# Kernel tuning notes

Hardware: AMD Instinct MI355X
Metric: run time of the kernel (lower is better)

## Reference

```python
import jax, jax.numpy as jnp
import numpy as np

N, E = 100_000, 800_000
D = 100   # memory_dim (in_channels)
T = 100   # time_dim
H, C = 2, 50  # heads, per-head out channels (embedding_dim = H*C = 100)
M = 172   # msg_dim
ED = M + T  # edge_dim for TransformerConv


def setup_inputs() -> dict:
    key = jax.random.key(0)
    ks = jax.random.split(key, 16)
    w = lambda k, shp: jax.random.normal(k, shp, jnp.float32) * 0.05
    return {
        "x": jax.random.normal(ks[0], (N, D), jnp.float32),
        "last_update": jax.random.uniform(ks[1], (N,), jnp.float32, 0.0, 1000.0),
        "t": jax.random.uniform(ks[2], (E,), jnp.float32, 0.0, 1000.0),
        "msg": jax.random.normal(ks[3], (E, M), jnp.float32),
        # TimeEncoder: Linear(1, T) followed by cos
        "Wt": w(ks[4], (T,)), "bt": w(ks[5], (T,)),
        # TransformerConv linears (lin_edge has no bias in PyG)
        "Wq": w(ks[6], (D, H * C)), "bq": w(ks[7], (H * C,)),
        "Wk": w(ks[8], (D, H * C)), "bk": w(ks[9], (H * C,)),
        "Wv": w(ks[10], (D, H * C)), "bv": w(ks[11], (H * C,)),
        "We": w(ks[12], (ED, H * C)),
        "Ws": w(ks[13], (D, H * C)), "bs": w(ks[14], (H * C,)),
        "edge_index": jax.random.randint(ks[15], (2, E), 0, N, jnp.int32),
    }


def reference(x, last_update, t, msg, Wt, bt, Wq, bq, Wk, bk, Wv, bv, We, Ws, bs, edge_index):
    n = x.shape[0]
    scale = 1.0 / np.sqrt(C).astype(np.float32)
    src, dst = edge_index[0], edge_index[1]

    # rel_t = last_update[src] - t; time encoding = cos(Linear(rel_t))
    rel_t = last_update[src] - t                              # [E]
    rel_enc = jnp.cos(rel_t[:, None] * Wt[None, :] + bt)      # [E, T]
    edge_attr = jnp.concatenate([rel_enc, msg], axis=-1)      # [E, ED]

    # per-node projections, gathered per edge (cheaper than per-edge GEMM)
    q = (x @ Wq + bq).reshape(n, H, C)
    k = (x @ Wk + bk).reshape(n, H, C)
    v = (x @ Wv + bv).reshape(n, H, C)
    e = (edge_attr @ We).reshape(-1, H, C)                    # [E, H, C]

    k_e = k[src] + e
    alpha = jnp.einsum('ehc,ehc->eh', q[dst], k_e) * scale    # [E, H]

    # segment softmax over incoming edges of each destination node
    amax = jax.ops.segment_max(alpha, dst, num_segments=n)
    amax = jnp.where(jnp.isfinite(amax), amax, 0.0)
    ex = jnp.exp(alpha - amax[dst])
    denom = jax.ops.segment_sum(ex, dst, num_segments=n)
    attn = ex / denom[dst]                                    # [E, H]

    out = jax.ops.segment_sum(attn[:, :, None] * (v[src] + e), dst, num_segments=n)
    return out.reshape(n, H * C) + x @ Ws + bs                # [N, H*C]
```

## Files before the change

### kernel.cpp

```cpp
#include <hip/hip_runtime.h>
#include <math.h>

#define N_NODES 100000
#define N_EDGES 800000
#define D_IN    100
#define T_DIM   100
#define M_DIM   172
#define ED_DIM  272
#define HC      100
#define CHD     50

#define NPB 32
__global__ __launch_bounds__(256) void node_proj(
    const float* __restrict__ x,
    const float* __restrict__ Wq, const float* __restrict__ bq,
    const float* __restrict__ Wk, const float* __restrict__ bk,
    const float* __restrict__ Wv, const float* __restrict__ bv,
    const float* __restrict__ Ws, const float* __restrict__ bs,
    float* __restrict__ qo, float* __restrict__ ko,
    float* __restrict__ vo, float* __restrict__ so)
{
    __shared__ __align__(16) float xs[NPB][D_IN];
    __shared__ float Wl[D_IN * HC];
    const int t  = threadIdx.x;
    const int n0 = blockIdx.x * NPB;

    for (int idx = t; idx < NPB * D_IN; idx += 256) {
        int n = idx / D_IN, i = idx - n * D_IN;
        xs[n][i] = x[(size_t)(n0 + n) * D_IN + i];
    }

    const float* Wm[4] = {Wq, Wk, Wv, Ws};
    const float* bm[4] = {bq, bk, bv, bs};
    float*       om[4] = {qo, ko, vo, so};

    const int ng   = t >> 6;
    const int lane = t & 63;
    const bool has2 = (lane + 64) < HC;

    for (int m = 0; m < 4; ++m) {
        __syncthreads();
        const float* W = Wm[m];
        for (int idx = t; idx < D_IN * HC; idx += 256) Wl[idx] = W[idx];
        __syncthreads();

        float acc[8][2];
        #pragma unroll
        for (int j = 0; j < 8; ++j) { acc[j][0] = 0.f; acc[j][1] = 0.f; }

        for (int i = 0; i < D_IN; i += 4) {
            float4 xv[8];
            #pragma unroll
            for (int j = 0; j < 8; ++j)
                xv[j] = *(const float4*)&xs[ng * 8 + j][i];
            #pragma unroll
            for (int kk = 0; kk < 4; ++kk) {
                float w0 = Wl[(i + kk) * HC + lane];
                float w1 = has2 ? Wl[(i + kk) * HC + lane + 64] : 0.f;
                #pragma unroll
                for (int j = 0; j < 8; ++j) {
                    float xx = ((const float*)&xv[j])[kk];
                    acc[j][0] += xx * w0;
                    acc[j][1] += xx * w1;
                }
            }
        }
        float b0 = bm[m][lane];
        float b1 = has2 ? bm[m][lane + 64] : 0.f;
        #pragma unroll
        for (int j = 0; j < 8; ++j) {
            size_t n = (size_t)(n0 + ng * 8 + j);
            om[m][n * HC + lane] = acc[j][0] + b0;
            if (has2) om[m][n * HC + lane + 64] = acc[j][1] + b1;
        }
    }
}

#define ET   64
#define ASTR 276
__global__ __launch_bounds__(320) void edge_pass(
    const float* __restrict__ last_update, const float* __restrict__ tarr,
    const float* __restrict__ msg,
    const float* __restrict__ Wt, const float* __restrict__ bt,
    const float* __restrict__ We,
    const int* __restrict__ ei,
    const float* __restrict__ qv, const float* __restrict__ kv,
    const float* __restrict__ vv,
    float* __restrict__ out_num, float* __restrict__ denom)
{
    __shared__ __align__(16) float a[ET * ASTR];
    __shared__ float rel[ET];
    __shared__ int   src_s[ET], dst_s[ET];
    __shared__ float ap[ET][2];
    __shared__ float exs[ET][2];

    const int t   = threadIdx.x;
    const int e0g = blockIdx.x * ET;

    if (t < ET) {
        int s = ei[e0g + t];
        int d = ei[N_EDGES + e0g + t];
        src_s[t] = s; dst_s[t] = d;
        rel[t] = last_update[s] - tarr[e0g + t];
    }
    if (t < 2 * ET) ap[t >> 1][t & 1] = 0.f;
    __syncthreads();

    for (int idx = t; idx < ET * T_DIM; idx += 320) {
        int e = idx / T_DIM, i = idx - e * T_DIM;
        a[e * ASTR + i] = __cosf(rel[e] * Wt[i] + bt[i]);
    }
    for (int idx = t; idx < ET * M_DIM; idx += 320) {
        int e = idx / M_DIM, j = idx - e * M_DIM;
        a[e * ASTR + T_DIM + j] = msg[(size_t)(e0g + e) * M_DIM + j];
    }
    __syncthreads();

    const int eq = t / 20, cq = t - eq * 20;
    const int e0 = eq * 4, c0 = cq * 5;
    const int head = cq / 10;

    float acc[4][5];
    #pragma unroll
    for (int j = 0; j < 4; ++j)
        #pragma unroll
        for (int c = 0; c < 5; ++c) acc[j][c] = 0.f;

    for (int k = 0; k < ED_DIM; k += 4) {
        float4 av[4];
        #pragma unroll
        for (int j = 0; j < 4; ++j)
            av[j] = *(const float4*)&a[(e0 + j) * ASTR + k];
        #pragma unroll
        for (int kk = 0; kk < 4; ++kk) {
            float w[5];
            #pragma unroll
            for (int c = 0; c < 5; ++c)
                w[c] = We[(k + kk) * HC + c0 + c];
            #pragma unroll
            for (int j = 0; j < 4; ++j) {
                float aval = ((const float*)&av[j])[kk];
                #pragma unroll
                for (int c = 0; c < 5; ++c)
                    acc[j][c] += aval * w[c];
            }
        }
    }

    #pragma unroll
    for (int j = 0; j < 4; ++j) {
        int e = e0 + j;
        int s = src_s[e], d = dst_s[e];
        float p = 0.f;
        #pragma unroll
        for (int c = 0; c < 5; ++c) {
            float qc = qv[(size_t)d * HC + c0 + c];
            float kc = kv[(size_t)s * HC + c0 + c];
            p += qc * (kc + acc[j][c]);
        }
        atomicAdd(&ap[e][head], p);
    }
    __syncthreads();

    if (t < 2 * ET) {
        int e = t >> 1, h = t & 1;
        float alpha = ap[e][h] * 0.14142135623730950488f;
        float ex = __expf(alpha);
        exs[e][h] = ex;
        atomicAdd(&denom[(size_t)dst_s[e] * 2 + h], ex);
    }
    __syncthreads();

    #pragma unroll
    for (int j = 0; j < 4; ++j) {
        int e = e0 + j;
        int s = src_s[e], d = dst_s[e];
        float ex = exs[e][head];
        #pragma unroll
        for (int c = 0; c < 5; ++c) {
            int ch = c0 + c;
            float val = ex * (vv[(size_t)s * HC + ch] + acc[j][c]);
            atomicAdd(&out_num[(size_t)d * HC + ch], val);
        }
    }
}

__global__ __launch_bounds__(256) void finalize(
    const float* __restrict__ out_num, const float* __restrict__ denom,
    const float* __restrict__ s, float* __restrict__ out)
{
    int idx = blockIdx.x * 256 + threadIdx.x;
    if (idx >= N_NODES * HC) return;
    int n = idx / HC, ch = idx - n * HC, h = ch / CHD;
    float d = denom[n * 2 + h];
    float v = (d > 0.f) ? out_num[idx] / d : 0.f;
    out[idx] = v + s[idx];
}

extern "C" void kernel_launch(void* const* d_in, const int* in_sizes, int n_in,
                              void* d_out, int out_size, void* d_ws, size_t ws_size,
                              hipStream_t stream)
{
    const float* x           = (const float*)d_in[0];
    const float* last_update = (const float*)d_in[1];
    const float* t           = (const float*)d_in[2];
    const float* msg         = (const float*)d_in[3];
    const float* Wt          = (const float*)d_in[4];
    const float* bt          = (const float*)d_in[5];
    const float* Wq          = (const float*)d_in[6];
    const float* bq          = (const float*)d_in[7];
    const float* Wk          = (const float*)d_in[8];
    const float* bk          = (const float*)d_in[9];
    const float* Wv          = (const float*)d_in[10];
    const float* bv          = (const float*)d_in[11];
    const float* We          = (const float*)d_in[12];
    const float* Ws          = (const float*)d_in[13];
    const float* bs          = (const float*)d_in[14];
    const int*   ei          = (const int*)d_in[15];

    float* ws      = (float*)d_ws;
    float* qo      = ws;
    float* ko      = qo + 10000000;
    float* vo      = ko + 10000000;
    float* so      = vo + 10000000;
    float* out_num = so + 10000000;
    float* denom   = out_num + 10000000;

    hipMemsetAsync(out_num, 0, (size_t)(10000000 + 200000) * sizeof(float), stream);

    node_proj<<<N_NODES / NPB, 256, 0, stream>>>(
        x, Wq, bq, Wk, bk, Wv, bv, Ws, bs, qo, ko, vo, so);

    edge_pass<<<N_EDGES / ET, 320, 0, stream>>>(
        last_update, t, msg, Wt, bt, We, ei, qo, ko, vo, out_num, denom);

    finalize<<<(N_NODES * HC + 255) / 256, 256, 0, stream>>>(
        out_num, denom, so, (float*)d_out);
}
```

Measured before the change: 3.299 ms.

## Chunk edge-attr LDS tile over K and split node projections across grid

The edge kernel now stages the 272-wide edge-attribute tile in four 68-column chunks, so the LDS footprint per block drops from about 70KB to about 19KB. This lets more blocks reside per CU, at the cost of extra barriers per chunk. The node projection kernel now takes one of the four weight matrices per blockIdx.y instead of looping over all four in each block. That adds parallelism and removes the serial reload loop, but x is now read four times.

New measurement: 2.994 ms. 1.1x faster.

```diff
diff --git a/kernel.cpp b/kernel.cpp
--- a/kernel.cpp
+++ b/kernel.cpp
@@ -25,59 +25,59 @@
     const int t  = threadIdx.x;
     const int n0 = blockIdx.x * NPB;
 
+    const float* W; const float* b; float* o;
+    switch (blockIdx.y) {
+        case 0: W = Wq; b = bq; o = qo; break;
+        case 1: W = Wk; b = bk; o = ko; break;
+        case 2: W = Wv; b = bv; o = vo; break;
+        default: W = Ws; b = bs; o = so; break;
+    }
+
     for (int idx = t; idx < NPB * D_IN; idx += 256) {
         int n = idx / D_IN, i = idx - n * D_IN;
         xs[n][i] = x[(size_t)(n0 + n) * D_IN + i];
     }
-
-    const float* Wm[4] = {Wq, Wk, Wv, Ws};
-    const float* bm[4] = {bq, bk, bv, bs};
-    float*       om[4] = {qo, ko, vo, so};
+    for (int idx = t; idx < D_IN * HC; idx += 256) Wl[idx] = W[idx];
+    __syncthreads();
 
     const int ng   = t >> 6;
     const int lane = t & 63;
     const bool has2 = (lane + 64) < HC;
 
-    for (int m = 0; m < 4; ++m) {
-        __syncthreads();
-        const float* W = Wm[m];
-        for (int idx = t; idx < D_IN * HC; idx += 256) Wl[idx] = W[idx];
-        __syncthreads();
-
-        float acc[8][2];
-        #pragma unroll
-        for (int j = 0; j < 8; ++j) { acc[j][0] = 0.f; acc[j][1] = 0.f; }
-
-        for (int i = 0; i < D_IN; i += 4) {
-            float4 xv[8];
+    float acc[8][2];
+    #pragma unroll
+    for (int j = 0; j < 8; ++j) { acc[j][0] = 0.f; acc[j][1] = 0.f; }
+
+    for (int i = 0; i < D_IN; i += 4) {
+        float4 xv[8];
+        #pragma unroll
+        for (int j = 0; j < 8; ++j)
+            xv[j] = *(const float4*)&xs[ng * 8 + j][i];
+        #pragma unroll
+        for (int kk = 0; kk < 4; ++kk) {
+            float w0 = Wl[(i + kk) * HC + lane];
+            float w1 = has2 ? Wl[(i + kk) * HC + lane + 64] : 0.f;
             #pragma unroll
-            for (int j = 0; j < 8; ++j)
-                xv[j] = *(const float4*)&xs[ng * 8 + j][i];
-            #pragma unroll
-            for (int kk = 0; kk < 4; ++kk) {
-                float w0 = Wl[(i + kk) * HC + lane];
-                float w1 = has2 ? Wl[(i + kk) * HC + lane + 64] : 0.f;
-                #pragma unroll
-                for (int j = 0; j < 8; ++j) {
-                    float xx = ((const float*)&xv[j])[kk];
-                    acc[j][0] += xx * w0;
-                    acc[j][1] += xx * w1;
-                }
+            for (int j = 0; j < 8; ++j) {
+                float xx = ((const float*)&xv[j])[kk];
+                acc[j][0] += xx * w0;
+                acc[j][1] += xx * w1;
             }
         }
-        float b0 = bm[m][lane];
-        float b1 = has2 ? bm[m][lane + 64] : 0.f;
-        #pragma unroll
-        for (int j = 0; j < 8; ++j) {
-            size_t n = (size_t)(n0 + ng * 8 + j);
-            om[m][n * HC + lane] = acc[j][0] + b0;
-            if (has2) om[m][n * HC + lane + 64] = acc[j][1] + b1;
-        }
+    }
+    float b0 = b[lane];
+    float b1 = has2 ? b[lane + 64] : 0.f;
+    #pragma unroll
+    for (int j = 0; j < 8; ++j) {
+        size_t n = (size_t)(n0 + ng * 8 + j);
+        o[n * HC + lane] = acc[j][0] + b0;
+        if (has2) o[n * HC + lane + 64] = acc[j][1] + b1;
     }
 }
 
 #define ET   64
-#define ASTR 276
+#define KC   68
+#define KSTR 76
 __global__ __launch_bounds__(320) void edge_pass(
     const float* __restrict__ last_update, const float* __restrict__ tarr,
     const float* __restrict__ msg,
@@ -88,7 +88,7 @@
     const float* __restrict__ vv,
     float* __restrict__ out_num, float* __restrict__ denom)
 {
-    __shared__ __align__(16) float a[ET * ASTR];
+    __shared__ __align__(16) float a[ET * KSTR];
     __shared__ float rel[ET];
     __shared__ int   src_s[ET], dst_s[ET];
     __shared__ float ap[ET][2];
@@ -104,17 +104,6 @@
         rel[t] = last_update[s] - tarr[e0g + t];
     }
     if (t < 2 * ET) ap[t >> 1][t & 1] = 0.f;
-    __syncthreads();
-
-    for (int idx = t; idx < ET * T_DIM; idx += 320) {
-        int e = idx / T_DIM, i = idx - e * T_DIM;
-        a[e * ASTR + i] = __cosf(rel[e] * Wt[i] + bt[i]);
-    }
-    for (int idx = t; idx < ET * M_DIM; idx += 320) {
-        int e = idx / M_DIM, j = idx - e * M_DIM;
-        a[e * ASTR + T_DIM + j] = msg[(size_t)(e0g + e) * M_DIM + j];
-    }
-    __syncthreads();
 
     const int eq = t / 20, cq = t - eq * 20;
     const int e0 = eq * 4, c0 = cq * 5;
@@ -126,23 +115,37 @@
         #pragma unroll
         for (int c = 0; c < 5; ++c) acc[j][c] = 0.f;
 
-    for (int k = 0; k < ED_DIM; k += 4) {
-        float4 av[4];
-        #pragma unroll
-        for (int j = 0; j < 4; ++j)
-            av[j] = *(const float4*)&a[(e0 + j) * ASTR + k];
-        #pragma unroll
-        for (int kk = 0; kk < 4; ++kk) {
-            float w[5];
+    for (int ch = 0; ch < 4; ++ch) {
+        const int g0 = ch * KC;
+        __syncthreads();
+        for (int idx = t; idx < ET * KC; idx += 320) {
+            int e = idx / KC, c = idx - e * KC;
+            int g = g0 + c;
+            float v;
+            if (g < T_DIM) v = __cosf(rel[e] * Wt[g] + bt[g]);
+            else           v = msg[(size_t)(e0g + e) * M_DIM + (g - T_DIM)];
+            a[e * KSTR + c] = v;
+        }
+        __syncthreads();
+
+        for (int k = 0; k < KC; k += 4) {
+            float4 av[4];
             #pragma unroll
-            for (int c = 0; c < 5; ++c)
-                w[c] = We[(k + kk) * HC + c0 + c];
+            for (int j = 0; j < 4; ++j)
+                av[j] = *(const float4*)&a[(e0 + j) * KSTR + k];
             #pragma unroll
-            for (int j = 0; j < 4; ++j) {
-                float aval = ((const float*)&av[j])[kk];
+            for (int kk = 0; kk < 4; ++kk) {
+                float w[5];
                 #pragma unroll
                 for (int c = 0; c < 5; ++c)
-                    acc[j][c] += aval * w[c];
+                    w[c] = We[(g0 + k + kk) * HC + c0 + c];
+                #pragma unroll
+                for (int j = 0; j < 4; ++j) {
+                    float aval = ((const float*)&av[j])[kk];
+                    #pragma unroll
+                    for (int c = 0; c < 5; ++c)
+                        acc[j][c] += aval * w[c];
+                }
             }
         }
     }
@@ -178,9 +181,9 @@
         float ex = exs[e][head];
         #pragma unroll
         for (int c = 0; c < 5; ++c) {
-            int ch = c0 + c;
-            float val = ex * (vv[(size_t)s * HC + ch] + acc[j][c]);
-            atomicAdd(&out_num[(size_t)d * HC + ch], val);
+            int chn = c0 + c;
+            float val = ex * (vv[(size_t)s * HC + chn] + acc[j][c]);
+            atomicAdd(&out_num[(size_t)d * HC + chn], val);
         }
     }
 }
@@ -228,7 +231,8 @@
 
     hipMemsetAsync(out_num, 0, (size_t)(10000000 + 200000) * sizeof(float), stream);
 
-    node_proj<<<N_NODES / NPB, 256, 0, stream>>>(
+    dim3 npgrid(N_NODES / NPB, 4);
+    node_proj<<<npgrid, 256, 0, stream>>>(
         x, Wq, bq, Wk, bk, Wv, bv, Ws, bs, qo, ko, vo, so);
 
     edge_pass<<<N_EDGES / ET, 320, 0, stream>>>(
```
